# Kernel tuning notes

Measured on AMD Instinct MI355X. Metric: run time of the kernel, lower is better.

Reference implementation:

```python
import jax, jax.numpy as jnp
import numpy as np

N, E, IN, H, OUT = 100000, 1600000, 128, 128, 64


def setup_inputs() -> dict:
    key = jax.random.key(0)
    ks = jax.random.split(key, 6)
    glorot = lambda k, i, o: jax.random.normal(k, (i, o), jnp.float32) * np.float32(np.sqrt(2.0 / (i + o)))
    return dict(
        x=jax.random.normal(ks[0], (N, IN), jnp.float32),
        edge_index=jax.random.randint(ks[1], (2, E), 0, N, dtype=jnp.int64 if jax.config.jax_enable_x64 else jnp.int32),
        W1=glorot(ks[2], IN, H), b1=jnp.zeros((H,), jnp.float32),
        W2=glorot(ks[3], H, H), b2=jnp.zeros((H,), jnp.float32),
        W3=glorot(ks[4], H, OUT), b3=jnp.zeros((OUT,), jnp.float32),
    )


def _gcn_norm(edge_index, num_nodes):
    # add self loops with weight 1.0 (GCNConv add_self_loops=True, edge_weight=None -> ones)
    loop = jnp.arange(num_nodes, dtype=edge_index.dtype)
    src = jnp.concatenate([edge_index[0], loop])
    dst = jnp.concatenate([edge_index[1], loop])
    ew = jnp.ones(src.shape, jnp.float32)
    deg = jax.ops.segment_sum(ew, dst, num_segments=num_nodes)  # in-degree on dst
    dinv = jnp.where(deg > 0, jax.lax.rsqrt(deg), 0.0)
    norm = dinv[src] * ew * dinv[dst]  # [E+N]
    return src, dst, norm


def _conv(x, src, dst, norm, W, b):
    h = x @ W                                        # linear transform first (GCNConv order)
    msg = h[src] * norm[:, None]                     # gather + scale, [E+N, F]
    agg = jax.ops.segment_sum(msg, dst, num_segments=x.shape[0])  # scatter-add
    return agg + b


def reference(x, edge_index, W1, b1, W2, b2, W3, b3):
    # eval-mode forward: dropout is identity
    src, dst, norm = _gcn_norm(edge_index, x.shape[0])  # same graph -> norm shared across layers
    h = jax.nn.relu(_conv(x, src, dst, norm, W1, b1))
    h = jax.nn.relu(_conv(h, src, dst, norm, W2, b2))
    h = _conv(h, src, dst, norm, W3, b3)
    return jax.nn.log_softmax(h, axis=-1)
```

## Files before the change

kernel.cpp:

```cpp
#include <hip/hip_runtime.h>

typedef unsigned int u32;
typedef unsigned short u16;
typedef unsigned char u8;
typedef long i64;
typedef __attribute__((ext_vector_type(8))) short short8;
typedef __attribute__((ext_vector_type(4))) float f32x4;
typedef __attribute__((ext_vector_type(2))) float f32x2;

#define MAXBIN 1024
#define SORT_TPB 1024

__device__ inline u16 f2bf(float f) {
    u32 u = __builtin_bit_cast(u32, f);
    u32 r = (u + 0x7fffu + ((u >> 16) & 1u)) >> 16;
    return (u16)r;
}

__device__ inline f32x4 mfma_fp8(uint2 a, uint2 b, f32x4 c) {
    return __builtin_amdgcn_mfma_f32_16x16x32_fp8_fp8(
        __builtin_bit_cast(i64, a), __builtin_bit_cast(i64, b), c, 0, 0, 0);
}

__device__ inline int permP(int p) {
    return ((p >> 5) << 5) + ((p & 3) << 3) + ((p >> 2) & 7);
}

__global__ __launch_bounds__(SORT_TPB) void k_bhist(const int* __restrict__ ei, int E, int W,
                                                    int* __restrict__ binTot, int NBIN) {
    __shared__ int h[MAXBIN];
    int tid = threadIdx.x;
    for (int i = tid; i < NBIN; i += SORT_TPB) h[i] = 0;
    __syncthreads();
    int s = blockIdx.x * W, e = min(E, s + W);
    for (int j = s + tid; j < e; j += SORT_TPB) atomicAdd(&h[ei[E + j] >> 7], 1);
    __syncthreads();
    for (int i = tid; i < NBIN; i += SORT_TPB) {
        int v = h[i];
        if (v) atomicAdd(&binTot[i], v);
    }
}

__global__ void k_bscan(const int* __restrict__ binTot, int NBIN,
                        int* __restrict__ binStart, int* __restrict__ binCur) {
    __shared__ int wsum[4];
    int t = threadIdx.x;
    int base = t * 4;
    int v0 = (base + 0 < NBIN) ? binTot[base + 0] : 0;
    int v1 = (base + 1 < NBIN) ? binTot[base + 1] : 0;
    int v2 = (base + 2 < NBIN) ? binTot[base + 2] : 0;
    int v3 = (base + 3 < NBIN) ? binTot[base + 3] : 0;
    int s = v0 + v1 + v2 + v3;
    int lane = t & 63, wv = t >> 6;
    int isc = s;
    for (int d = 1; d < 64; d <<= 1) { int o = __shfl_up(isc, d, 64); if (lane >= d) isc += o; }
    if (lane == 63) wsum[wv] = isc;
    __syncthreads();
    int woff = 0;
    for (int w = 0; w < wv; w++) woff += wsum[w];
    int run = woff + isc - s;
    if (base + 0 < NBIN) { binStart[base + 0] = run; binCur[base + 0] = run; } run += v0;
    if (base + 1 < NBIN) { binStart[base + 1] = run; binCur[base + 1] = run; } run += v1;
    if (base + 2 < NBIN) { binStart[base + 2] = run; binCur[base + 2] = run; } run += v2;
    if (base + 3 < NBIN) { binStart[base + 3] = run; binCur[base + 3] = run; }
    if (t == 255) binStart[NBIN] = wsum[0] + wsum[1] + wsum[2] + wsum[3];
}

__global__ __launch_bounds__(SORT_TPB) void k_bscatter(const int* __restrict__ ei, int E, int W,
                                                       int* __restrict__ binCur,
                                                       u32* __restrict__ binned, int NBIN) {
    __shared__ int lh[MAXBIN];
    __shared__ int lb[MAXBIN];
    int tid = threadIdx.x;
    for (int i = tid; i < NBIN; i += SORT_TPB) lh[i] = 0;
    __syncthreads();
    int s = blockIdx.x * W, e = min(E, s + W);
    for (int j = s + tid; j < e; j += SORT_TPB) atomicAdd(&lh[ei[E + j] >> 7], 1);
    __syncthreads();
    for (int i = tid; i < NBIN; i += SORT_TPB) {
        int h = lh[i];
        lb[i] = h ? atomicAdd(&binCur[i], h) : 0;
    }
    __syncthreads();
    for (int i = tid; i < NBIN; i += SORT_TPB) lh[i] = 0;
    __syncthreads();
    for (int j = s + tid; j < e; j += SORT_TPB) {
        int d = ei[E + j];
        int b = d >> 7;
        int r = atomicAdd(&lh[b], 1);
        binned[lb[b] + r] = ((u32)ei[j] << 7) | (u32)(d & 127);
    }
}

__global__ __launch_bounds__(256) void k_bcsr(const u32* __restrict__ binned,
                                              const int* __restrict__ binStart,
                                              int N, int E, int* __restrict__ offs,
                                              float* __restrict__ dinv,
                                              int* __restrict__ csr, int NBIN) {
    __shared__ int cnt[128];
    __shared__ int off[128];
    __shared__ int tot;
    int b = blockIdx.x;
    int tid = threadIdx.x;
    int dLo = b << 7;
    int nd = min(128, N - dLo);
    int e0 = binStart[b], e1 = binStart[b + 1];
    if (tid < 128) cnt[tid] = 0;
    __syncthreads();
    for (int j = e0 + tid; j < e1; j += 256) atomicAdd(&cnt[binned[j] & 127u], 1);
    __syncthreads();
    int c = (tid < 128) ? cnt[tid] : 0;
    int lane = tid & 63;
    int isc = c;
    for (int d = 1; d < 64; d <<= 1) { int o = __shfl_up(isc, d, 64); if (lane >= d) isc += o; }
    if (tid == 63) tot = isc;
    __syncthreads();
    int add = (tid >= 64 && tid < 128) ? tot : 0;
    if (tid < 128) off[tid] = add + isc - c;
    __syncthreads();
    if (tid < nd) {
        offs[dLo + tid] = e0 + off[tid];
        dinv[dLo + tid] = rsqrtf((float)(c + 1));
    }
    if (b == NBIN - 1 && tid == 0) offs[N] = E;
    if (tid < 128) cnt[tid] = 0;
    __syncthreads();
    for (int j = e0 + tid; j < e1; j += 256) {
        u32 v = binned[j];
        int d7 = (int)(v & 127u);
        int r = atomicAdd(&cnt[d7], 1);
        csr[e0 + off[d7] + r] = (int)(v >> 7);
    }
}

__global__ void k_wtall(const float* __restrict__ W1, const float* __restrict__ W2,
                        const float* __restrict__ W3, u16* __restrict__ wt1,
                        u16* __restrict__ wt2, u16* __restrict__ wt3) {
    int idx = blockIdx.x * 256 + threadIdx.x;
    if (idx < 16384) {
        int k = idx >> 7, m = idx & 127;
        wt1[m * 128 + k] = f2bf(W1[idx]);
    } else if (idx < 32768) {
        int i = idx - 16384, p = i >> 7, m = i & 127;
        wt2[m * 128 + p] = f2bf(W2[permP(p) * 128 + m]);
    } else if (idx < 40960) {
        int i = idx - 32768, p = i >> 6, m = i & 63;
        wt3[m * 128 + p] = f2bf(W3[permP(p) * 64 + m]);
    }
}

template <int M, bool F32IN>
__global__ __launch_bounds__(256) void k_gemm(const void* __restrict__ xin,
                                              const u16* __restrict__ wt,
                                              const float* __restrict__ dinv,
                                              u8* __restrict__ g8, int N) {
    constexpr int K = 128;
    constexpr int LDK = 136;
    __shared__ u16 lwt[M * LDK];
    int tid = threadIdx.x;
    const uint4* wsrc = (const uint4*)wt;
#pragma unroll
    for (int c = tid; c < M * K / 8; c += 256) {
        int row = c >> 4, kc = c & 15;
        *(uint4*)&lwt[row * LDK + kc * 8] = wsrc[c];
    }
    __syncthreads();
    int lane = tid & 63, wv = tid >> 6;
    int node = blockIdx.x * 64 + wv * 16 + (lane & 15);
    int nodec = min(node, N - 1);
    int kr = (lane >> 4) * 8;
    f32x4 acc[M / 16];
#pragma unroll
    for (int t = 0; t < M / 16; t++) acc[t] = (f32x4){0.f, 0.f, 0.f, 0.f};
#pragma unroll
    for (int ks = 0; ks < 4; ks++) {
        short8 bfr;
        if (F32IN) {
            const float* xr = (const float*)xin + (size_t)nodec * K + ks * 32 + kr;
            float4 fa = *(const float4*)xr;
            float4 fb = *(const float4*)(xr + 4);
            bfr = (short8){(short)f2bf(fa.x), (short)f2bf(fa.y), (short)f2bf(fa.z),
                           (short)f2bf(fa.w), (short)f2bf(fb.x), (short)f2bf(fb.y),
                           (short)f2bf(fb.z), (short)f2bf(fb.w)};
        } else {
            bfr = *(const short8*)((const u16*)xin + (size_t)nodec * K + ks * 32 + kr);
        }
#pragma unroll
        for (int t = 0; t < M / 16; t++) {
            short8 afr = *(const short8*)&lwt[(t * 16 + (lane & 15)) * LDK + ks * 32 + kr];
            acc[t] = __builtin_amdgcn_mfma_f32_16x16x32_bf16(afr, bfr, acc[t], 0, 0, 0);
        }
    }
    if (node < N) {
        float dv16 = dinv[node] * 16.0f;
        int r0 = (lane >> 4) * 4;
#pragma unroll
        for (int t = 0; t < M / 16; t++) {
            u32 w = __builtin_amdgcn_cvt_pk_fp8_f32(acc[t][0] * dv16, acc[t][1] * dv16, 0, false);
            w = __builtin_amdgcn_cvt_pk_fp8_f32(acc[t][2] * dv16, acc[t][3] * dv16, w, true);
            *(u32*)(g8 + (size_t)node * M + t * 16 + r0) = w;
        }
    }
}

__global__ __launch_bounds__(256) void k_agg128(const u8* __restrict__ g8,
                                                const int* __restrict__ offs,
                                                const int* __restrict__ csr,
                                                const float* __restrict__ dinv,
                                                const float* __restrict__ bias,
                                                u16* __restrict__ hout, int N) {
    int wid = (blockIdx.x * 256 + threadIdx.x) >> 6;
    if (wid >= N) return;
    int lane = threadIdx.x & 63;
    int q = lane >> 4;
    int f = lane & 15;
    int s = offs[wid], e = offs[wid + 1];
    uint2 bsel;
    bsel.x = (f < 4) ? (0x38u << (8 * f)) : 0u;
    bsel.y = (f >= 4 && f < 8) ? (0x38u << (8 * (f - 4))) : 0u;
    const u8* gf = g8 + f * 8;
    f32x4 ac0 = {0.f, 0.f, 0.f, 0.f}, ac1 = ac0, ac2 = ac0, ac3 = ac0;
    {
        uint2 w = make_uint2(0u, 0u);
        if (q == 0) w = *(const uint2*)(gf + ((u32)wid << 7));
        ac0 = mfma_fp8(w, bsel, ac0);
    }
    int em1 = e - 1;
    for (int j = s; j < e; j += 16) {
        int i0 = j + q, i1 = j + 4 + q, i2 = j + 8 + q, i3 = j + 12 + q;
        int s0 = csr[min(i0, em1)];
        int s1 = csr[min(i1, em1)];
        int s2 = csr[min(i2, em1)];
        int s3 = csr[min(i3, em1)];
        uint2 w0 = *(const uint2*)(gf + ((u32)s0 << 7));
        uint2 w1 = *(const uint2*)(gf + ((u32)s1 << 7));
        uint2 w2 = *(const uint2*)(gf + ((u32)s2 << 7));
        uint2 w3 = *(const uint2*)(gf + ((u32)s3 << 7));
        if (i0 >= e) { w0.x = 0u; w0.y = 0u; }
        if (i1 >= e) { w1.x = 0u; w1.y = 0u; }
        if (i2 >= e) { w2.x = 0u; w2.y = 0u; }
        if (i3 >= e) { w3.x = 0u; w3.y = 0u; }
        ac0 = mfma_fp8(w0, bsel, ac0);
        ac1 = mfma_fp8(w1, bsel, ac1);
        ac2 = mfma_fp8(w2, bsel, ac2);
        ac3 = mfma_fp8(w3, bsel, ac3);
    }
    f32x4 a = (ac0 + ac1) + (ac2 + ac3);
    int jn = lane & 15, fq = lane >> 4;
    if (jn < 8) {
        float sc = dinv[wid] * 0.0625f;
        u32 o0, o1;
        {
            float v0 = fmaxf(fmaf(a[0], sc, bias[(4 * fq + 0) * 8 + jn]), 0.f);
            float v1 = fmaxf(fmaf(a[1], sc, bias[(4 * fq + 1) * 8 + jn]), 0.f);
            o0 = (u32)f2bf(v0) | ((u32)f2bf(v1) << 16);
        }
        {
            float v2 = fmaxf(fmaf(a[2], sc, bias[(4 * fq + 2) * 8 + jn]), 0.f);
            float v3 = fmaxf(fmaf(a[3], sc, bias[(4 * fq + 3) * 8 + jn]), 0.f);
            o1 = (u32)f2bf(v2) | ((u32)f2bf(v3) << 16);
        }
        *(uint2*)&hout[(size_t)wid * 128 + fq * 32 + jn * 4] = make_uint2(o0, o1);
    }
}

__global__ __launch_bounds__(256) void k_agg64(const u8* __restrict__ g8,
                                               const int* __restrict__ offs,
                                               const int* __restrict__ csr,
                                               const float* __restrict__ dinv,
                                               const float* __restrict__ bias,
                                               float* __restrict__ out, int N) {
    __shared__ float sm[4][64];
    int wid = (blockIdx.x * 256 + threadIdx.x) >> 6;
    if (wid >= N) return;
    int lane = threadIdx.x & 63;
    int wv = (int)(threadIdx.x >> 6);
    int q = lane >> 4;
    int f = lane & 15;
    bool frow = (f < 8);
    int s = offs[wid], e = offs[wid + 1];
    uint2 bsel;
    bsel.x = (f < 4) ? (0x38u << (8 * f)) : 0u;
    bsel.y = (f >= 4 && f < 8) ? (0x38u << (8 * (f - 4))) : 0u;
    const u8* gf = g8 + f * 8;
    f32x4 ac0 = {0.f, 0.f, 0.f, 0.f}, ac1 = ac0, ac2 = ac0, ac3 = ac0;
    {
        uint2 w = make_uint2(0u, 0u);
        if (q == 0 && frow) w = *(const uint2*)(gf + ((u32)wid << 6));
        ac0 = mfma_fp8(w, bsel, ac0);
    }
    int em1 = e - 1;
    for (int j = s; j < e; j += 16) {
        int i0 = j + q, i1 = j + 4 + q, i2 = j + 8 + q, i3 = j + 12 + q;
        int s0 = csr[min(i0, em1)];
        int s1 = csr[min(i1, em1)];
        int s2 = csr[min(i2, em1)];
        int s3 = csr[min(i3, em1)];
        uint2 w0 = make_uint2(0u, 0u), w1 = w0, w2 = w0, w3 = w0;
        if (frow) {
            w0 = *(const uint2*)(gf + ((u32)s0 << 6));
            w1 = *(const uint2*)(gf + ((u32)s1 << 6));
            w2 = *(const uint2*)(gf + ((u32)s2 << 6));
            w3 = *(const uint2*)(gf + ((u32)s3 << 6));
        }
        if (i0 >= e) { w0.x = 0u; w0.y = 0u; }
        if (i1 >= e) { w1.x = 0u; w1.y = 0u; }
        if (i2 >= e) { w2.x = 0u; w2.y = 0u; }
        if (i3 >= e) { w3.x = 0u; w3.y = 0u; }
        ac0 = mfma_fp8(w0, bsel, ac0);
        ac1 = mfma_fp8(w1, bsel, ac1);
        ac2 = mfma_fp8(w2, bsel, ac2);
        ac3 = mfma_fp8(w3, bsel, ac3);
    }
    f32x4 a = (ac0 + ac1) + (ac2 + ac3);
    int jn = lane & 15, fq = lane >> 4;
    bool act = (jn < 8) && (fq < 2);
    if (act) {
        float sc = dinv[wid] * 0.0625f;
        float v0 = fmaf(a[0], sc, bias[(4 * fq + 0) * 8 + jn]);
        float v1 = fmaf(a[1], sc, bias[(4 * fq + 1) * 8 + jn]);
        float v2 = fmaf(a[2], sc, bias[(4 * fq + 2) * 8 + jn]);
        float v3 = fmaf(a[3], sc, bias[(4 * fq + 3) * 8 + jn]);
        float m = fmaxf(fmaxf(v0, v1), fmaxf(v2, v3));
        m = fmaxf(m, __shfl_xor(m, 1, 64));
        m = fmaxf(m, __shfl_xor(m, 2, 64));
        m = fmaxf(m, __shfl_xor(m, 4, 64));
        m = fmaxf(m, __shfl_xor(m, 16, 64));
        float ss = __expf(v0 - m) + __expf(v1 - m) + __expf(v2 - m) + __expf(v3 - m);
        ss += __shfl_xor(ss, 1, 64);
        ss += __shfl_xor(ss, 2, 64);
        ss += __shfl_xor(ss, 4, 64);
        ss += __shfl_xor(ss, 16, 64);
        float lg = m + __logf(ss);
        sm[wv][(4 * fq + 0) * 8 + jn] = v0 - lg;
        sm[wv][(4 * fq + 1) * 8 + jn] = v1 - lg;
        sm[wv][(4 * fq + 2) * 8 + jn] = v2 - lg;
        sm[wv][(4 * fq + 3) * 8 + jn] = v3 - lg;
    }
    if (lane < 16) {
        float4 ov = *(float4*)&sm[wv][lane * 4];
        *(float4*)&out[(size_t)wid * 64 + lane * 4] = ov;
    }
}

extern "C" void kernel_launch(void* const* d_in, const int* in_sizes, int n_in,
                              void* d_out, int out_size, void* d_ws, size_t ws_size,
                              hipStream_t stream) {
    const float* x  = (const float*)d_in[0];
    const int*   ei = (const int*)d_in[1];
    const float* W1 = (const float*)d_in[2];
    const float* b1 = (const float*)d_in[3];
    const float* W2 = (const float*)d_in[4];
    const float* b2 = (const float*)d_in[5];
    const float* W3 = (const float*)d_in[6];
    const float* b3 = (const float*)d_in[7];
    const int N = in_sizes[0] / 128;
    const int E = in_sizes[1] / 2;
    const int NBIN = (N + 127) >> 7;

    char* ws = (char*)d_ws;
    size_t o = 0;
    auto alloc = [&](size_t bytes) -> char* {
        char* p = ws + o;
        o += (bytes + 255) & ~(size_t)255;
        return p;
    };
    int*   binTot = (int*)alloc((size_t)MAXBIN * 4);
    int*   binSt  = (int*)alloc((size_t)(MAXBIN + 1) * 4);
    int*   binCur = (int*)alloc((size_t)MAXBIN * 4);
    float* dinv   = (float*)alloc((size_t)N * 4);
    int*   offs   = (int*)alloc((size_t)(N + 1) * 4);
    int*   csr    = (int*)alloc((size_t)E * 4);
    u16*   wt1    = (u16*)alloc(128 * 128 * 2);
    u16*   wt2    = (u16*)alloc(128 * 128 * 2);
    u16*   wt3    = (u16*)alloc(64 * 128 * 2);
    u8*    g8     = (u8*)alloc((size_t)N * 128);
    u16*   hbuf   = (u16*)alloc((size_t)N * 128 * 2);
    u32*   binned = (u32*)hbuf;
    float* outp   = (float*)d_out;

    hipMemsetAsync(binTot, 0, (size_t)MAXBIN * 4, stream);
    int W256 = (E + 255) / 256;
    k_bhist<<<256, SORT_TPB, 0, stream>>>(ei, E, W256, binTot, NBIN);
    k_bscan<<<1, 256, 0, stream>>>(binTot, NBIN, binSt, binCur);
    k_bscatter<<<256, SORT_TPB, 0, stream>>>(ei, E, W256, binCur, binned, NBIN);
    k_bcsr<<<NBIN, 256, 0, stream>>>(binned, binSt, N, E, offs, dinv, csr, NBIN);
    k_wtall<<<(40960 + 255) / 256, 256, 0, stream>>>(W1, W2, W3, wt1, wt2, wt3);

    int gG = (N + 63) / 64;
    int gA = (int)(((size_t)N * 64 + 255) / 256);

    k_gemm<128, true ><<<gG, 256, 0, stream>>>(x,    wt1, dinv, g8, N);
    k_agg128<<<gA, 256, 0, stream>>>(g8, offs, csr, dinv, b1, hbuf, N);
    k_gemm<128, false><<<gG, 256, 0, stream>>>(hbuf, wt2, dinv, g8, N);
    k_agg128<<<gA, 256, 0, stream>>>(g8, offs, csr, dinv, b2, hbuf, N);
    k_gemm<64,  false><<<gG, 256, 0, stream>>>(hbuf, wt3, dinv, g8, N);
    k_agg64<<<gA, 256, 0, stream>>>(g8, offs, csr, dinv, b3, outp, N);
}
```

Baseline: 308.7 us.

## Pad CSR rows to multiples of sixteen with sentinel zero row

Builds the CSR with each node's neighbor list padded to a multiple of 16. The self-loop is stored inline and padding slots point to a zeroed sentinel row N in g8. This removes the bounds clamping, masking and separate self-loop MFMA from the aggregation loops, and the 64-wide aggregation now uses all 16 lane groups with two accumulators plus a cross-half shuffle. The cost is extra CSR memory and padding writes, plus wasted gathers on padded slots. Correctness depends on the per-bin slack being large enough for the padding.

```diff
diff --git a/kernel.cpp b/kernel.cpp
--- a/kernel.cpp
+++ b/kernel.cpp
@@ -6,10 +6,10 @@
 typedef long i64;
 typedef __attribute__((ext_vector_type(8))) short short8;
 typedef __attribute__((ext_vector_type(4))) float f32x4;
-typedef __attribute__((ext_vector_type(2))) float f32x2;
 
 #define MAXBIN 1024
 #define SORT_TPB 1024
+#define BINSLACK 2048
 
 __device__ inline u16 f2bf(float f) {
     u32 u = __builtin_bit_cast(u32, f);
@@ -77,6 +77,7 @@
     int s = blockIdx.x * W, e = min(E, s + W);
     for (int j = s + tid; j < e; j += SORT_TPB) atomicAdd(&lh[ei[E + j] >> 7], 1);
     __syncthreads();
+    for (int i = tid; i < SORT_TPB ? 0 : 0; i++) {}
     for (int i = tid; i < NBIN; i += SORT_TPB) {
         int h = lh[i];
         lb[i] = h ? atomicAdd(&binCur[i], h) : 0;
@@ -95,6 +96,7 @@
 __global__ __launch_bounds__(256) void k_bcsr(const u32* __restrict__ binned,
                                               const int* __restrict__ binStart,
                                               int N, int E, int* __restrict__ offs,
+                                              int* __restrict__ ends,
                                               float* __restrict__ dinv,
                                               int* __restrict__ csr, int NBIN) {
     __shared__ int cnt[128];
@@ -105,31 +107,36 @@
     int dLo = b << 7;
     int nd = min(128, N - dLo);
     int e0 = binStart[b], e1 = binStart[b + 1];
+    int pbase = e0 + b * BINSLACK;
+    int pend = e1 + (b + 1) * BINSLACK;
     if (tid < 128) cnt[tid] = 0;
     __syncthreads();
     for (int j = e0 + tid; j < e1; j += 256) atomicAdd(&cnt[binned[j] & 127u], 1);
     __syncthreads();
     int c = (tid < 128) ? cnt[tid] : 0;
+    int pc = (tid < 128) ? ((c + 16) & ~15) : 0;
     int lane = tid & 63;
-    int isc = c;
+    int isc = pc;
     for (int d = 1; d < 64; d <<= 1) { int o = __shfl_up(isc, d, 64); if (lane >= d) isc += o; }
     if (tid == 63) tot = isc;
     __syncthreads();
     int add = (tid >= 64 && tid < 128) ? tot : 0;
-    if (tid < 128) off[tid] = add + isc - c;
+    if (tid < 128) off[tid] = add + isc - pc;
+    for (int j = pbase + tid; j < pend; j += 256) csr[j] = N;
     __syncthreads();
     if (tid < nd) {
-        offs[dLo + tid] = e0 + off[tid];
+        offs[dLo + tid] = pbase + off[tid];
+        ends[dLo + tid] = pbase + off[tid] + pc;
         dinv[dLo + tid] = rsqrtf((float)(c + 1));
-    }
-    if (b == NBIN - 1 && tid == 0) offs[N] = E;
+        csr[pbase + off[tid] + c] = dLo + tid;
+    }
     if (tid < 128) cnt[tid] = 0;
     __syncthreads();
     for (int j = e0 + tid; j < e1; j += 256) {
         u32 v = binned[j];
         int d7 = (int)(v & 127u);
         int r = atomicAdd(&cnt[d7], 1);
-        csr[e0 + off[d7] + r] = (int)(v >> 7);
+        csr[pbase + off[d7] + r] = (int)(v >> 7);
     }
 }
 
@@ -158,6 +165,8 @@
     constexpr int LDK = 136;
     __shared__ u16 lwt[M * LDK];
     int tid = threadIdx.x;
+    if (blockIdx.x == 0 && tid < M / 16)
+        *(uint4*)(g8 + (size_t)N * M + (size_t)tid * 16) = make_uint4(0u, 0u, 0u, 0u);
     const uint4* wsrc = (const uint4*)wt;
 #pragma unroll
     for (int c = tid; c < M * K / 8; c += 256) {
@@ -205,6 +214,7 @@
 
 __global__ __launch_bounds__(256) void k_agg128(const u8* __restrict__ g8,
                                                 const int* __restrict__ offs,
+                                                const int* __restrict__ ends,
                                                 const int* __restrict__ csr,
                                                 const float* __restrict__ dinv,
                                                 const float* __restrict__ bias,
@@ -214,32 +224,21 @@
     int lane = threadIdx.x & 63;
     int q = lane >> 4;
     int f = lane & 15;
-    int s = offs[wid], e = offs[wid + 1];
+    int s = offs[wid], e = ends[wid];
     uint2 bsel;
     bsel.x = (f < 4) ? (0x38u << (8 * f)) : 0u;
     bsel.y = (f >= 4 && f < 8) ? (0x38u << (8 * (f - 4))) : 0u;
     const u8* gf = g8 + f * 8;
     f32x4 ac0 = {0.f, 0.f, 0.f, 0.f}, ac1 = ac0, ac2 = ac0, ac3 = ac0;
-    {
-        uint2 w = make_uint2(0u, 0u);
-        if (q == 0) w = *(const uint2*)(gf + ((u32)wid << 7));
-        ac0 = mfma_fp8(w, bsel, ac0);
-    }
-    int em1 = e - 1;
     for (int j = s; j < e; j += 16) {
-        int i0 = j + q, i1 = j + 4 + q, i2 = j + 8 + q, i3 = j + 12 + q;
-        int s0 = csr[min(i0, em1)];
-        int s1 = csr[min(i1, em1)];
-        int s2 = csr[min(i2, em1)];
-        int s3 = csr[min(i3, em1)];
+        int s0 = csr[j + q];
+        int s1 = csr[j + 4 + q];
+        int s2 = csr[j + 8 + q];
+        int s3 = csr[j + 12 + q];
         uint2 w0 = *(const uint2*)(gf + ((u32)s0 << 7));
         uint2 w1 = *(const uint2*)(gf + ((u32)s1 << 7));
         uint2 w2 = *(const uint2*)(gf + ((u32)s2 << 7));
         uint2 w3 = *(const uint2*)(gf + ((u32)s3 << 7));
-        if (i0 >= e) { w0.x = 0u; w0.y = 0u; }
-        if (i1 >= e) { w1.x = 0u; w1.y = 0u; }
-        if (i2 >= e) { w2.x = 0u; w2.y = 0u; }
-        if (i3 >= e) { w3.x = 0u; w3.y = 0u; }
         ac0 = mfma_fp8(w0, bsel, ac0);
         ac1 = mfma_fp8(w1, bsel, ac1);
         ac2 = mfma_fp8(w2, bsel, ac2);
@@ -266,6 +265,7 @@
 
 __global__ __launch_bounds__(256) void k_agg64(const u8* __restrict__ g8,
                                                const int* __restrict__ offs,
+                                               const int* __restrict__ ends,
                                                const int* __restrict__ csr,
                                                const float* __restrict__ dinv,
                                                const float* __restrict__ bias,
@@ -277,42 +277,24 @@
     int wv = (int)(threadIdx.x >> 6);
     int q = lane >> 4;
     int f = lane & 15;
-    bool frow = (f < 8);
-    int s = offs[wid], e = offs[wid + 1];
+    int qq = q + ((f >> 3) << 2);
+    int s = offs[wid], e = ends[wid];
     uint2 bsel;
     bsel.x = (f < 4) ? (0x38u << (8 * f)) : 0u;
     bsel.y = (f >= 4 && f < 8) ? (0x38u << (8 * (f - 4))) : 0u;
-    const u8* gf = g8 + f * 8;
-    f32x4 ac0 = {0.f, 0.f, 0.f, 0.f}, ac1 = ac0, ac2 = ac0, ac3 = ac0;
-    {
-        uint2 w = make_uint2(0u, 0u);
-        if (q == 0 && frow) w = *(const uint2*)(gf + ((u32)wid << 6));
-        ac0 = mfma_fp8(w, bsel, ac0);
-    }
-    int em1 = e - 1;
+    const u8* gf = g8 + (f & 7) * 8;
+    f32x4 ac0 = {0.f, 0.f, 0.f, 0.f}, ac1 = ac0;
     for (int j = s; j < e; j += 16) {
-        int i0 = j + q, i1 = j + 4 + q, i2 = j + 8 + q, i3 = j + 12 + q;
-        int s0 = csr[min(i0, em1)];
-        int s1 = csr[min(i1, em1)];
-        int s2 = csr[min(i2, em1)];
-        int s3 = csr[min(i3, em1)];
-        uint2 w0 = make_uint2(0u, 0u), w1 = w0, w2 = w0, w3 = w0;
-        if (frow) {
-            w0 = *(const uint2*)(gf + ((u32)s0 << 6));
-            w1 = *(const uint2*)(gf + ((u32)s1 << 6));
-            w2 = *(const uint2*)(gf + ((u32)s2 << 6));
-            w3 = *(const uint2*)(gf + ((u32)s3 << 6));
-        }
-        if (i0 >= e) { w0.x = 0u; w0.y = 0u; }
-        if (i1 >= e) { w1.x = 0u; w1.y = 0u; }
-        if (i2 >= e) { w2.x = 0u; w2.y = 0u; }
-        if (i3 >= e) { w3.x = 0u; w3.y = 0u; }
-        ac0 = mfma_fp8(w0, bsel, ac0);
-        ac1 = mfma_fp8(w1, bsel, ac1);
-        ac2 = mfma_fp8(w2, bsel, ac2);
-        ac3 = mfma_fp8(w3, bsel, ac3);
-    }
-    f32x4 a = (ac0 + ac1) + (ac2 + ac3);
+        int sA = csr[j + qq];
+        int sB = csr[j + 8 + qq];
+        uint2 wA = *(const uint2*)(gf + ((u32)sA << 6));
+        uint2 wB = *(const uint2*)(gf + ((u32)sB << 6));
+        ac0 = mfma_fp8(wA, bsel, ac0);
+        ac1 = mfma_fp8(wB, bsel, ac1);
+    }
+    f32x4 a = ac0 + ac1;
+#pragma unroll
+    for (int r = 0; r < 4; r++) a[r] += __shfl_xor(a[r], 32, 64);
     int jn = lane & 15, fq = lane >> 4;
     bool act = (jn < 8) && (fq < 2);
     if (act) {
@@ -369,12 +351,13 @@
     int*   binSt  = (int*)alloc((size_t)(MAXBIN + 1) * 4);
     int*   binCur = (int*)alloc((size_t)MAXBIN * 4);
     float* dinv   = (float*)alloc((size_t)N * 4);
-    int*   offs   = (int*)alloc((size_t)(N + 1) * 4);
-    int*   csr    = (int*)alloc((size_t)E * 4);
+    int*   offs   = (int*)alloc((size_t)N * 4);
+    int*   endsA  = (int*)alloc((size_t)N * 4);
+    int*   csr    = (int*)alloc(((size_t)E + (size_t)NBIN * BINSLACK + 64) * 4);
     u16*   wt1    = (u16*)alloc(128 * 128 * 2);
     u16*   wt2    = (u16*)alloc(128 * 128 * 2);
     u16*   wt3    = (u16*)alloc(64 * 128 * 2);
-    u8*    g8     = (u8*)alloc((size_t)N * 128);
+    u8*    g8     = (u8*)alloc(((size_t)N + 1) * 128);
     u16*   hbuf   = (u16*)alloc((size_t)N * 128 * 2);
     u32*   binned = (u32*)hbuf;
     float* outp   = (float*)d_out;
@@ -384,16 +367,16 @@
     k_bhist<<<256, SORT_TPB, 0, stream>>>(ei, E, W256, binTot, NBIN);
     k_bscan<<<1, 256, 0, stream>>>(binTot, NBIN, binSt, binCur);
     k_bscatter<<<256, SORT_TPB, 0, stream>>>(ei, E, W256, binCur, binned, NBIN);
-    k_bcsr<<<NBIN, 256, 0, stream>>>(binned, binSt, N, E, offs, dinv, csr, NBIN);
+    k_bcsr<<<NBIN, 256, 0, stream>>>(binned, binSt, N, E, offs, endsA, dinv, csr, NBIN);
     k_wtall<<<(40960 + 255) / 256, 256, 0, stream>>>(W1, W2, W3, wt1, wt2, wt3);
 
     int gG = (N + 63) / 64;
     int gA = (int)(((size_t)N * 64 + 255) / 256);
 
     k_gemm<128, true ><<<gG, 256, 0, stream>>>(x,    wt1, dinv, g8, N);
-    k_agg128<<<gA, 256, 0, stream>>>(g8, offs, csr, dinv, b1, hbuf, N);
+    k_agg128<<<gA, 256, 0, stream>>>(g8, offs, endsA, csr, dinv, b1, hbuf, N);
     k_gemm<128, false><<<gG, 256, 0, stream>>>(hbuf, wt2, dinv, g8, N);
-    k_agg128<<<gA, 256, 0, stream>>>(g8, offs, csr, dinv, b2, hbuf, N);
+    k_agg128<<<gA, 256, 0, stream>>>(g8, offs, endsA, csr, dinv, b2, hbuf, N);
     k_gemm<64,  false><<<gG, 256, 0, stream>>>(hbuf, wt3, dinv, g8, N);
-    k_agg64<<<gA, 256, 0, stream>>>(g8, offs, csr, dinv, b3, outp, N);
-}
+    k_agg64<<<gA, 256, 0, stream>>>(g8, offs, endsA, csr, dinv, b3, outp, N);
+}
```

After: 309.8 us. Within noise of the previous version (+0.4%).
